# Kernel tuning notes

Measured on AMD Instinct MI355X. Metric: run time of the kernel, lower is better.

Reference implementation:

```python
import jax, jax.numpy as jnp
import numpy as np

# ---- config (from init_kwargs) ----
IMG_SIZE = (4096.0, 4096.0)
MAP_SIZE = (256, 256)
BASE_SIZE = 16
RATIOS = np.array([0.5, 1.0, 2.0], dtype=np.float64)
SCALES = np.array([8.0, 16.0, 32.0], dtype=np.float64)
FEAT_STRIDE = 16
RPN_MIN_SIZE = 16.0
PRE_NMS_N = 12000
POST_NMS_N = 2000
NMS_THRESH = 0.7


def _generate_anchors():
    base = np.array([1, 1, BASE_SIZE, BASE_SIZE], dtype=np.float64) - 1
    w = base[2] - base[0] + 1
    h = base[3] - base[1] + 1
    cx = base[0] + 0.5 * (w - 1)
    cy = base[1] + 0.5 * (h - 1)
    size = w * h
    ws = np.round(np.sqrt(size / RATIOS))
    hs = np.round(ws * RATIOS)
    ratio_anchors = np.stack([cx - 0.5 * (ws - 1), cy - 0.5 * (hs - 1),
                              cx + 0.5 * (ws - 1), cy + 0.5 * (hs - 1)], axis=1)
    out = []
    for a in ratio_anchors:
        aw = a[2] - a[0] + 1
        ah = a[3] - a[1] + 1
        acx = a[0] + 0.5 * (aw - 1)
        acy = a[1] + 0.5 * (ah - 1)
        ws2 = aw * SCALES
        hs2 = ah * SCALES
        out.append(np.stack([acx - 0.5 * (ws2 - 1), acy - 0.5 * (hs2 - 1),
                             acx + 0.5 * (ws2 - 1), acy + 0.5 * (hs2 - 1)], axis=1))
    return np.concatenate(out, axis=0).astype(np.float32)  # [A=9, 4]


def _all_anchors():
    A = _generate_anchors()
    H, W = MAP_SIZE
    sx = np.arange(W) * FEAT_STRIDE
    sy = np.arange(H) * FEAT_STRIDE
    sx, sy = np.meshgrid(sx, sy)
    shifts = np.stack([sx.ravel(), sy.ravel(), sx.ravel(), sy.ravel()], axis=1).astype(np.float32)  # [K,4]
    return (shifts[:, None, :] + A[None, :, :]).reshape(-1, 4)  # [K*A, 4]


_ALL_ANCHORS = _all_anchors()  # [N, 4] constant


def setup_inputs() -> dict:
    key = jax.random.key(0)
    k1, k2 = jax.random.split(key)
    n = _ALL_ANCHORS.shape[0]
    delta = jax.random.normal(k1, (1, n, 4), dtype=jnp.float32) * 0.1
    score = jax.random.uniform(k2, (1, n, 2), dtype=jnp.float32)
    return {"delta": delta, "score": score}


def _proposal_forward(delta, score):
    anchors = jnp.asarray(_ALL_ANCHORS)  # [N,4]
    d = delta[0]                         # [N,4]
    s = score[0, :, 1]                   # [N]

    widths = anchors[:, 2] - anchors[:, 0] + 1.0
    heights = anchors[:, 3] - anchors[:, 1] + 1.0
    ctr_x = anchors[:, 0] + 0.5 * widths
    ctr_y = anchors[:, 1] + 0.5 * heights
    pcx = d[:, 0] * widths + ctr_x
    pcy = d[:, 1] * heights + ctr_y
    pw = jnp.exp(d[:, 2]) * widths
    ph = jnp.exp(d[:, 3]) * heights
    x0 = jnp.clip(pcx - 0.5 * pw, 0.0, IMG_SIZE[0])
    y0 = jnp.clip(pcy - 0.5 * ph, 0.0, IMG_SIZE[1])
    x1 = jnp.clip(pcx + 0.5 * pw, 0.0, IMG_SIZE[0])
    y1 = jnp.clip(pcy + 0.5 * ph, 0.0, IMG_SIZE[1])
    props = jnp.stack([x0, y0, x1, y1], axis=1)  # [N,4]

    # min-size filter: mask instead of dynamic gather (jit-friendly)
    w = props[:, 2] - props[:, 0]
    h = props[:, 3] - props[:, 1]
    valid = (w >= RPN_MIN_SIZE) & (h >= RPN_MIN_SIZE)
    s = jnp.where(valid, s, -jnp.inf)

    top_s, top_i = jax.lax.top_k(s, PRE_NMS_N)   # sorted descending
    boxes = props[top_i]                          # [PRE,4]

    # greedy NMS over score-sorted boxes, fixed POST_NMS_N iterations
    areas = (boxes[:, 2] - boxes[:, 0]) * (boxes[:, 3] - boxes[:, 1])
    alive0 = top_s > -jnp.inf

    def step(alive, _):
        i = jnp.argmax(jnp.where(alive, top_s, -jnp.inf))
        ok = alive[i]
        b = boxes[i]
        xx0 = jnp.maximum(b[0], boxes[:, 0])
        yy0 = jnp.maximum(b[1], boxes[:, 1])
        xx1 = jnp.minimum(b[2], boxes[:, 2])
        yy1 = jnp.minimum(b[3], boxes[:, 3])
        inter = jnp.maximum(xx1 - xx0, 0.0) * jnp.maximum(yy1 - yy0, 0.0)
        iou = inter / jnp.maximum(areas[i] + areas - inter, 1e-8)
        alive = alive & (iou <= NMS_THRESH)
        out = jnp.where(ok, b, jnp.zeros_like(b))  # zero-pad like tf.pad
        return alive, out

    _, selected = jax.lax.scan(step, alive0, None, length=POST_NMS_N)  # [POST,4]
    return selected[None]  # [1, POST_NMS_N, 4]


def reference(delta, score):
    return _proposal_forward(delta, score)
```

## Files before the change

### kernel.cpp

```cpp
#include <hip/hip_runtime.h>
#include <hip/hip_bf16.h>

#define N_ANCH   589824
#define NBLK     2304
#define TOPK     12000
#define KPAD     12032
#define NW       188
#define OUTN     2000
#define CAP      32768
#define NBIN     65536

typedef unsigned long long u64;

__constant__ float c_aw[9] = {184.f, 368.f, 736.f, 128.f, 256.f, 512.f,  88.f, 176.f, 352.f};
__constant__ float c_ah[9] = { 96.f, 192.f, 384.f, 128.f, 256.f, 512.f, 176.f, 352.f, 704.f};

__device__ __forceinline__ void decode_one(int i, const float4* __restrict__ delta,
                                           float4* box, bool* valid) {
#pragma clang fp contract(off)
    int a    = i % 9;
    int cell = i / 9;
    int gx = cell & 255;
    int gy = cell >> 8;
    float w = c_aw[a], h = c_ah[a];
    float cx = (float)gx * 16.0f + 8.0f;
    float cy = (float)gy * 16.0f + 8.0f;
    float4 d = delta[i];
    float pcx = d.x * w + cx;
    float pcy = d.y * h + cy;
    float pw  = expf(d.z) * w;
    float ph  = expf(d.w) * h;
    float x0 = fminf(fmaxf(pcx - 0.5f * pw, 0.f), 4096.f);
    float y0 = fminf(fmaxf(pcy - 0.5f * ph, 0.f), 4096.f);
    float x1 = fminf(fmaxf(pcx + 0.5f * pw, 0.f), 4096.f);
    float y1 = fminf(fmaxf(pcy + 0.5f * ph, 0.f), 4096.f);
    *box = make_float4(x0, y0, x1, y1);
    *valid = (x1 - x0 >= 16.f) && (y1 - y0 >= 16.f);
}

__global__ __launch_bounds__(256) void k_score(const float4* __restrict__ delta,
                                               const float2* __restrict__ score,
                                               unsigned* __restrict__ ukey,
                                               unsigned* __restrict__ hist,
                                               unsigned* __restrict__ ctrl) {
    int tid = threadIdx.x;
    int i = blockIdx.x * 256 + tid;
    float4 box; bool valid;
    decode_one(i, delta, &box, &valid);
    unsigned u = 0u;
    if (valid) {
        unsigned b = __float_as_uint(score[i].y);
        u = (b & 0x80000000u) ? ~b : (b | 0x80000000u);
    }
    ukey[i] = u;
    atomicAdd(&hist[u >> 16], 1u);

    __shared__ int lastf;
    __threadfence();
    __syncthreads();
    if (tid == 0) lastf = (atomicAdd(&ctrl[8], 1u) == (unsigned)(gridDim.x - 1)) ? 1 : 0;
    __syncthreads();
    if (!lastf) return;

    __shared__ unsigned ss[256];
    __shared__ int sc;
    unsigned csum = 0;
    const unsigned* hb = hist + tid * 256;
    #pragma unroll 8
    for (int k = 0; k < 256; ++k) csum += hb[k];
    ss[tid] = csum;
    if (tid == 0) sc = -1;
    __syncthreads();
    for (int d = 1; d < 256; d <<= 1) {
        unsigned v = (tid + d < 256) ? ss[tid + d] : 0u;
        __syncthreads();
        ss[tid] += v;
        __syncthreads();
    }
    unsigned nextS = (tid + 1 < 256) ? ss[tid + 1] : 0u;
    if (ss[tid] >= (unsigned)TOPK && nextS < (unsigned)TOPK) sc = tid;
    __syncthreads();
    if (tid == 0) {
        unsigned P = 0;
        int c = sc;
        if (c >= 0) {
            unsigned acc = (c + 1 < 256) ? ss[c + 1] : 0u;
            int b = 255;
            for (; b > 0; --b) {
                acc += hist[c * 256 + b];
                if (acc >= (unsigned)TOPK) break;
            }
            P = (unsigned)(c * 256 + b);
        }
        ctrl[0] = P;
    }
}

__global__ __launch_bounds__(256) void k_compact(const unsigned* __restrict__ ukey,
                                                 const unsigned* __restrict__ ctrl,
                                                 unsigned* __restrict__ cnt,
                                                 u64* __restrict__ cand) {
    unsigned P = ctrl[0];
    int i = blockIdx.x * 256 + threadIdx.x;
    unsigned u = ukey[i];
    bool pred = (u != 0u) && ((u >> 16) >= P);
    u64 m = __ballot(pred);
    if (m == 0ull) return;
    int lane = threadIdx.x & 63;
    int leader = __ffsll(m) - 1;
    unsigned base = 0;
    if (lane == leader) base = atomicAdd(cnt, (unsigned)__popcll(m));
    base = __shfl(base, leader);
    if (pred) {
        u64 below = m & ((1ull << lane) - 1ull);
        unsigned pos = base + (unsigned)__popcll(below);
        if (pos < CAP) cand[pos] = ((u64)u << 32) | (unsigned)(~i);
    }
}

__global__ __launch_bounds__(256) void k_rankdec(const u64* __restrict__ cand,
                                                 const unsigned* __restrict__ ctrl,
                                                 const float4* __restrict__ delta,
                                                 float4* __restrict__ sboxes) {
    unsigned cnt = ctrl[3];
    int C = (int)(cnt < (unsigned)CAP ? cnt : (unsigned)CAP);
    if ((int)(blockIdx.x * 256) >= C) return;
    int t = blockIdx.x * 256 + threadIdx.x;
    u64 mykey = (t < C) ? cand[t] : ~0ull;
    int rank = 0;
    __shared__ u64 tile[256];
    for (int j0 = 0; j0 < C; j0 += 256) {
        int j = j0 + threadIdx.x;
        tile[threadIdx.x] = (j < C) ? cand[j] : 0ull;
        __syncthreads();
        int lim = (C - j0 < 256) ? (C - j0) : 256;
        #pragma unroll 4
        for (int jj = 0; jj < lim; ++jj) rank += (tile[jj] > mykey) ? 1 : 0;
        __syncthreads();
    }
    if (t < C && rank < TOPK) {
        int idx = (int)(~(unsigned)mykey);
        float4 box; bool v;
        decode_one(idx, delta, &box, &v);
        sboxes[rank] = box;
    }
}

__global__ __launch_bounds__(64) void k_mask(const float4* __restrict__ sboxes,
                                             u64* __restrict__ mask) {
    int cb = blockIdx.x, rb = blockIdx.y;
    if (cb < rb) return;
    __shared__ float4 cbox[64];
    int tid = threadIdx.x;
    cbox[tid] = sboxes[cb * 64 + tid];
    __syncthreads();
    int r = rb * 64 + tid;
    float4 me = sboxes[r];
    float areaMe = (me.z - me.x) * (me.w - me.y);
    u64 bits = 0ull;
    for (int j = 0; j < 64; ++j) {
        float4 o = cbox[j];
        float xx0 = fmaxf(me.x, o.x);
        float yy0 = fmaxf(me.y, o.y);
        float xx1 = fminf(me.z, o.z);
        float yy1 = fminf(me.w, o.w);
        float iw = fmaxf(xx1 - xx0, 0.f);
        float ih = fmaxf(yy1 - yy0, 0.f);
        float inter = iw * ih;
        float areaO = (o.z - o.x) * (o.w - o.y);
        float denom = fmaxf(areaMe + areaO - inter, 1e-8f);
        float iou = inter / denom;
        if (iou > 0.7f && (cb * 64 + j) != r) bits |= (1ull << j);
    }
    mask[(size_t)r * NW + cb] = bits;
}

__global__ __launch_bounds__(256) void k_reduce(const float4* __restrict__ sboxes,
                                                const unsigned* __restrict__ ctrl,
                                                const u64* __restrict__ mask,
                                                float4* __restrict__ out) {
    int t = threadIdx.x;
    int lane = t & 63;
    int wave = t >> 6;
    unsigned cnt = ctrl[3];
    int C = (int)(cnt < (unsigned)CAP ? cnt : (unsigned)CAP);
    int nvalid = C < TOPK ? C : TOPK;
    int nblocks = (nvalid + 63) >> 6;

    __shared__ u64 diag[2][64];
    __shared__ u64 s_rw;
    __shared__ unsigned s_rows[64];
    __shared__ int s_kc;
    __shared__ int s_nkept;

    u64 removed_t = ~0ull;
    if (t < NW) {
        long long lo = (long long)t * 64;
        if (lo + 64 <= (long long)nvalid) removed_t = 0ull;
        else if (lo < (long long)nvalid)
            removed_t = ~((1ull << (unsigned)(nvalid - lo)) - 1ull);
    }
    if (t == 0) s_nkept = 0;
    if (wave == 3 && nblocks > 0) diag[0][lane] = mask[(size_t)lane * NW + 0];
    __syncthreads();

    for (int b = 0; b < nblocks; ++b) {
        int cur = b & 1;
        if (wave == 3 && b + 1 < nblocks)
            diag[cur ^ 1][lane] = mask[(size_t)((b + 1) * 64 + lane) * NW + (b + 1)];
        if (t == b) s_rw = removed_t;
        __syncthreads();

        if (wave == 0) {
            u64 dg = diag[cur][lane];
            u64 avail = ~s_rw;
            int nk = s_nkept;
            int budget = OUTN - nk;
            u64 keptmask = 0ull; int kc = 0;
            while (avail && kc < budget) {
                int j = __ffsll(avail) - 1;
                keptmask |= (1ull << j);
                ++kc;
                u64 dj = __shfl(dg, j);
                avail &= ~dj;
                avail &= ~(1ull << j);
            }
            if ((keptmask >> lane) & 1ull) {
                int p = (int)__popcll(keptmask & ((1ull << lane) - 1ull));
                s_rows[p] = (unsigned)(b * 64 + lane);
                out[nk + p] = sboxes[b * 64 + lane];
            }
            if (kc > 0) {
                int r0 = b * 64 + (__ffsll(keptmask) - 1);
                int kcp = (kc + 7) & ~7;
                if (lane >= kc && lane < kcp) s_rows[lane] = (unsigned)r0;
            }
            if (lane == 0) { s_kc = kc; s_nkept = nk + kc; }
        }
        __syncthreads();

        if (s_nkept >= OUTN) break;
        int kc = s_kc;
        if (kc > 0 && t < NW && t > b) {
            const u64* mt = mask + t;
            u64 acc = removed_t;
            int kcp = (kc + 7) & ~7;
            for (int i = 0; i < kcp; i += 8) {
                u64 a0 = mt[(size_t)s_rows[i + 0] * NW];
                u64 a1 = mt[(size_t)s_rows[i + 1] * NW];
                u64 a2 = mt[(size_t)s_rows[i + 2] * NW];
                u64 a3 = mt[(size_t)s_rows[i + 3] * NW];
                u64 a4 = mt[(size_t)s_rows[i + 4] * NW];
                u64 a5 = mt[(size_t)s_rows[i + 5] * NW];
                u64 a6 = mt[(size_t)s_rows[i + 6] * NW];
                u64 a7 = mt[(size_t)s_rows[i + 7] * NW];
                acc |= ((a0 | a1) | (a2 | a3)) | ((a4 | a5) | (a6 | a7));
            }
            removed_t = acc;
        }
    }

    int nk = s_nkept;
    float4 z = make_float4(0.f, 0.f, 0.f, 0.f);
    for (int p = nk + t; p < OUTN; p += 256) out[p] = z;
}

extern "C" void kernel_launch(void* const* d_in, const int* in_sizes, int n_in,
                              void* d_out, int out_size, void* d_ws, size_t ws_size,
                              hipStream_t stream) {
    const float4* delta = (const float4*)d_in[0];
    const float2* score = (const float2*)d_in[1];
    char* ws = (char*)d_ws;

    unsigned* ukey = (unsigned*)(ws + 0);
    unsigned* hist = (unsigned*)(ws + 2359296);
    u64*      cand = (u64*)(ws + 2359296);
    unsigned* ctrl = (unsigned*)(ws + 2621440);
    float4*   sbox = (float4*)(ws + 2621504);
    u64*      mask = (u64*)(ws + 2814016);

    hipMemsetAsync(ws + 2359296, 0, 262144 + 64, stream);
    hipMemsetAsync(ws + 2621504, 0, 192512, stream);

    k_score  <<<NBLK,     256, 0, stream>>>(delta, score, ukey, hist, ctrl);
    k_compact<<<NBLK,     256, 0, stream>>>(ukey, ctrl, ctrl + 3, cand);
    k_rankdec<<<CAP/256,  256, 0, stream>>>(cand, ctrl, delta, sbox);
    dim3 mgrid(NW, NW);
    k_mask   <<<mgrid,    64,  0, stream>>>(sbox, mask);
    k_reduce <<<1,        256, 0, stream>>>(sbox, ctrl, mask, (float4*)d_out);
}
```

Baseline: 1.037 ms.

## Split histogram threshold into own kernel, coarsen mask blocks, widen reduce unroll

Moves the last-block histogram scan out of k_score into a separate 1024-thread k_thresh kernel that reads the histogram with vectorized uint4 loads. This removes the per-block threadfence and atomic counter from k_score, at the cost of one extra launch. k_mask now has each block handle four column tiles, cutting launch count and skipped empty blocks. k_reduce unrolls its mask OR loop to 16 loads so more memory requests are in flight, but pads kept rows to multiples of 16, which can add redundant loads.

```diff
diff --git a/kernel.cpp b/kernel.cpp
--- a/kernel.cpp
+++ b/kernel.cpp
@@ -8,7 +8,6 @@
 #define NW       188
 #define OUTN     2000
 #define CAP      32768
-#define NBIN     65536
 
 typedef unsigned long long u64;
 
@@ -41,10 +40,8 @@
 __global__ __launch_bounds__(256) void k_score(const float4* __restrict__ delta,
                                                const float2* __restrict__ score,
                                                unsigned* __restrict__ ukey,
-                                               unsigned* __restrict__ hist,
-                                               unsigned* __restrict__ ctrl) {
-    int tid = threadIdx.x;
-    int i = blockIdx.x * 256 + tid;
+                                               unsigned* __restrict__ hist) {
+    int i = blockIdx.x * 256 + threadIdx.x;
     float4 box; bool valid;
     decode_one(i, delta, &box, &valid);
     unsigned u = 0u;
@@ -54,43 +51,43 @@
     }
     ukey[i] = u;
     atomicAdd(&hist[u >> 16], 1u);
-
-    __shared__ int lastf;
-    __threadfence();
-    __syncthreads();
-    if (tid == 0) lastf = (atomicAdd(&ctrl[8], 1u) == (unsigned)(gridDim.x - 1)) ? 1 : 0;
-    __syncthreads();
-    if (!lastf) return;
-
-    __shared__ unsigned ss[256];
+}
+
+__global__ __launch_bounds__(1024) void k_thresh(const unsigned* __restrict__ hist,
+                                                 unsigned* __restrict__ ctrl) {
+    __shared__ unsigned ss[1024];
     __shared__ int sc;
+    int tid = threadIdx.x;
+    const uint4* hb = (const uint4*)hist + tid * 16;
     unsigned csum = 0;
-    const unsigned* hb = hist + tid * 256;
-    #pragma unroll 8
-    for (int k = 0; k < 256; ++k) csum += hb[k];
+    #pragma unroll
+    for (int k = 0; k < 16; ++k) {
+        uint4 h = hb[k];
+        csum += h.x + h.y + h.z + h.w;
+    }
     ss[tid] = csum;
     if (tid == 0) sc = -1;
     __syncthreads();
-    for (int d = 1; d < 256; d <<= 1) {
-        unsigned v = (tid + d < 256) ? ss[tid + d] : 0u;
+    for (int d = 1; d < 1024; d <<= 1) {
+        unsigned v = (tid + d < 1024) ? ss[tid + d] : 0u;
         __syncthreads();
         ss[tid] += v;
         __syncthreads();
     }
-    unsigned nextS = (tid + 1 < 256) ? ss[tid + 1] : 0u;
+    unsigned nextS = (tid + 1 < 1024) ? ss[tid + 1] : 0u;
     if (ss[tid] >= (unsigned)TOPK && nextS < (unsigned)TOPK) sc = tid;
     __syncthreads();
     if (tid == 0) {
         unsigned P = 0;
         int c = sc;
         if (c >= 0) {
-            unsigned acc = (c + 1 < 256) ? ss[c + 1] : 0u;
-            int b = 255;
+            unsigned acc = (c + 1 < 1024) ? ss[c + 1] : 0u;
+            int b = 63;
             for (; b > 0; --b) {
-                acc += hist[c * 256 + b];
+                acc += hist[c * 64 + b];
                 if (acc >= (unsigned)TOPK) break;
             }
-            P = (unsigned)(c * 256 + b);
+            P = (unsigned)(c * 64 + b);
         }
         ctrl[0] = P;
     }
@@ -148,31 +145,37 @@
 
 __global__ __launch_bounds__(64) void k_mask(const float4* __restrict__ sboxes,
                                              u64* __restrict__ mask) {
-    int cb = blockIdx.x, rb = blockIdx.y;
-    if (cb < rb) return;
-    __shared__ float4 cbox[64];
+    int rb = blockIdx.y;
+    int cb0 = blockIdx.x * 4;
+    if (cb0 + 3 < rb) return;
     int tid = threadIdx.x;
-    cbox[tid] = sboxes[cb * 64 + tid];
-    __syncthreads();
     int r = rb * 64 + tid;
     float4 me = sboxes[r];
     float areaMe = (me.z - me.x) * (me.w - me.y);
-    u64 bits = 0ull;
-    for (int j = 0; j < 64; ++j) {
-        float4 o = cbox[j];
-        float xx0 = fmaxf(me.x, o.x);
-        float yy0 = fmaxf(me.y, o.y);
-        float xx1 = fminf(me.z, o.z);
-        float yy1 = fminf(me.w, o.w);
-        float iw = fmaxf(xx1 - xx0, 0.f);
-        float ih = fmaxf(yy1 - yy0, 0.f);
-        float inter = iw * ih;
-        float areaO = (o.z - o.x) * (o.w - o.y);
-        float denom = fmaxf(areaMe + areaO - inter, 1e-8f);
-        float iou = inter / denom;
-        if (iou > 0.7f && (cb * 64 + j) != r) bits |= (1ull << j);
-    }
-    mask[(size_t)r * NW + cb] = bits;
+    __shared__ float4 cbox[64];
+    for (int q = 0; q < 4; ++q) {
+        int cb = cb0 + q;
+        if (cb < rb) continue;
+        __syncthreads();
+        cbox[tid] = sboxes[cb * 64 + tid];
+        __syncthreads();
+        u64 bits = 0ull;
+        for (int j = 0; j < 64; ++j) {
+            float4 o = cbox[j];
+            float xx0 = fmaxf(me.x, o.x);
+            float yy0 = fmaxf(me.y, o.y);
+            float xx1 = fminf(me.z, o.z);
+            float yy1 = fminf(me.w, o.w);
+            float iw = fmaxf(xx1 - xx0, 0.f);
+            float ih = fmaxf(yy1 - yy0, 0.f);
+            float inter = iw * ih;
+            float areaO = (o.z - o.x) * (o.w - o.y);
+            float denom = fmaxf(areaMe + areaO - inter, 1e-8f);
+            float iou = inter / denom;
+            if (iou > 0.7f && (cb * 64 + j) != r) bits |= (1ull << j);
+        }
+        mask[(size_t)r * NW + cb] = bits;
+    }
 }
 
 __global__ __launch_bounds__(256) void k_reduce(const float4* __restrict__ sboxes,
@@ -232,7 +235,7 @@
             }
             if (kc > 0) {
                 int r0 = b * 64 + (__ffsll(keptmask) - 1);
-                int kcp = (kc + 7) & ~7;
+                int kcp = (kc + 15) & ~15;
                 if (lane >= kc && lane < kcp) s_rows[lane] = (unsigned)r0;
             }
             if (lane == 0) { s_kc = kc; s_nkept = nk + kc; }
@@ -244,17 +247,26 @@
         if (kc > 0 && t < NW && t > b) {
             const u64* mt = mask + t;
             u64 acc = removed_t;
-            int kcp = (kc + 7) & ~7;
-            for (int i = 0; i < kcp; i += 8) {
-                u64 a0 = mt[(size_t)s_rows[i + 0] * NW];
-                u64 a1 = mt[(size_t)s_rows[i + 1] * NW];
-                u64 a2 = mt[(size_t)s_rows[i + 2] * NW];
-                u64 a3 = mt[(size_t)s_rows[i + 3] * NW];
-                u64 a4 = mt[(size_t)s_rows[i + 4] * NW];
-                u64 a5 = mt[(size_t)s_rows[i + 5] * NW];
-                u64 a6 = mt[(size_t)s_rows[i + 6] * NW];
-                u64 a7 = mt[(size_t)s_rows[i + 7] * NW];
-                acc |= ((a0 | a1) | (a2 | a3)) | ((a4 | a5) | (a6 | a7));
+            int kcp = (kc + 15) & ~15;
+            for (int i = 0; i < kcp; i += 16) {
+                u64 a0  = mt[(size_t)s_rows[i + 0]  * NW];
+                u64 a1  = mt[(size_t)s_rows[i + 1]  * NW];
+                u64 a2  = mt[(size_t)s_rows[i + 2]  * NW];
+                u64 a3  = mt[(size_t)s_rows[i + 3]  * NW];
+                u64 a4  = mt[(size_t)s_rows[i + 4]  * NW];
+                u64 a5  = mt[(size_t)s_rows[i + 5]  * NW];
+                u64 a6  = mt[(size_t)s_rows[i + 6]  * NW];
+                u64 a7  = mt[(size_t)s_rows[i + 7]  * NW];
+                u64 a8  = mt[(size_t)s_rows[i + 8]  * NW];
+                u64 a9  = mt[(size_t)s_rows[i + 9]  * NW];
+                u64 a10 = mt[(size_t)s_rows[i + 10] * NW];
+                u64 a11 = mt[(size_t)s_rows[i + 11] * NW];
+                u64 a12 = mt[(size_t)s_rows[i + 12] * NW];
+                u64 a13 = mt[(size_t)s_rows[i + 13] * NW];
+                u64 a14 = mt[(size_t)s_rows[i + 14] * NW];
+                u64 a15 = mt[(size_t)s_rows[i + 15] * NW];
+                acc |= (((a0 | a1) | (a2 | a3)) | ((a4 | a5) | (a6 | a7)))
+                     | (((a8 | a9) | (a10 | a11)) | ((a12 | a13) | (a14 | a15)));
             }
             removed_t = acc;
         }
@@ -282,10 +294,11 @@
     hipMemsetAsync(ws + 2359296, 0, 262144 + 64, stream);
     hipMemsetAsync(ws + 2621504, 0, 192512, stream);
 
-    k_score  <<<NBLK,     256, 0, stream>>>(delta, score, ukey, hist, ctrl);
-    k_compact<<<NBLK,     256, 0, stream>>>(ukey, ctrl, ctrl + 3, cand);
-    k_rankdec<<<CAP/256,  256, 0, stream>>>(cand, ctrl, delta, sbox);
-    dim3 mgrid(NW, NW);
-    k_mask   <<<mgrid,    64,  0, stream>>>(sbox, mask);
-    k_reduce <<<1,        256, 0, stream>>>(sbox, ctrl, mask, (float4*)d_out);
-}
+    k_score  <<<NBLK,    256,  0, stream>>>(delta, score, ukey, hist);
+    k_thresh <<<1,       1024, 0, stream>>>(hist, ctrl);
+    k_compact<<<NBLK,    256,  0, stream>>>(ukey, ctrl, ctrl + 3, cand);
+    k_rankdec<<<CAP/256, 256,  0, stream>>>(cand, ctrl, delta, sbox);
+    dim3 mgrid(47, NW);
+    k_mask   <<<mgrid,   64,   0, stream>>>(sbox, mask);
+    k_reduce <<<1,       256,  0, stream>>>(sbox, ctrl, mask, (float4*)d_out);
+}
```

Measured after the change: 985.1 us. 1.05x faster.

## Two-pass LDS radix histogram, column-major NMS mask, and barrier-light reduce loop

Applied to the files above, without the earlier changes.

Replaces the 65536-bin global-atomic histogram and last-block threshold search with two 256-bin passes that aggregate counts in shared memory first, adding a k_hist2 kernel. Each block of k_compact recomputes the threshold from the two histograms. The NMS mask becomes column-major, and each k_mask block computes four column tiles. k_reduce runs the intra-block greedy pass with ballot in all waves, so it needs one barrier per block instead of two, and it prefetches the kept-row mask words into registers. The cost is an extra launch and redundant prefix scans in every compact block.

```diff
diff --git a/kernel.cpp b/kernel.cpp
--- a/kernel.cpp
+++ b/kernel.cpp
@@ -8,7 +8,6 @@
 #define NW       188
 #define OUTN     2000
 #define CAP      32768
-#define NBIN     65536
 
 typedef unsigned long long u64;
 
@@ -41,9 +40,11 @@
 __global__ __launch_bounds__(256) void k_score(const float4* __restrict__ delta,
                                                const float2* __restrict__ score,
                                                unsigned* __restrict__ ukey,
-                                               unsigned* __restrict__ hist,
-                                               unsigned* __restrict__ ctrl) {
+                                               unsigned* __restrict__ hist1) {
+    __shared__ unsigned lh[256];
     int tid = threadIdx.x;
+    lh[tid] = 0u;
+    __syncthreads();
     int i = blockIdx.x * 256 + tid;
     float4 box; bool valid;
     decode_one(i, delta, &box, &valid);
@@ -53,23 +54,22 @@
         u = (b & 0x80000000u) ? ~b : (b | 0x80000000u);
     }
     ukey[i] = u;
-    atomicAdd(&hist[u >> 16], 1u);
-
-    __shared__ int lastf;
-    __threadfence();
-    __syncthreads();
-    if (tid == 0) lastf = (atomicAdd(&ctrl[8], 1u) == (unsigned)(gridDim.x - 1)) ? 1 : 0;
-    __syncthreads();
-    if (!lastf) return;
-
+    atomicAdd(&lh[u >> 24], 1u);
+    __syncthreads();
+    unsigned c = lh[tid];
+    if (c) atomicAdd(&hist1[tid], c);
+}
+
+__global__ __launch_bounds__(256) void k_hist2(const unsigned* __restrict__ ukey,
+                                               const unsigned* __restrict__ hist1,
+                                               unsigned* __restrict__ hist2) {
     __shared__ unsigned ss[256];
-    __shared__ int sc;
-    unsigned csum = 0;
-    const unsigned* hb = hist + tid * 256;
-    #pragma unroll 8
-    for (int k = 0; k < 256; ++k) csum += hb[k];
-    ss[tid] = csum;
-    if (tid == 0) sc = -1;
+    __shared__ unsigned lh[256];
+    __shared__ unsigned s_b1;
+    int tid = threadIdx.x;
+    ss[tid] = hist1[tid];
+    lh[tid] = 0u;
+    if (tid == 0) s_b1 = 0u;
     __syncthreads();
     for (int d = 1; d < 256; d <<= 1) {
         unsigned v = (tid + d < 256) ? ss[tid + d] : 0u;
@@ -77,36 +77,62 @@
         ss[tid] += v;
         __syncthreads();
     }
-    unsigned nextS = (tid + 1 < 256) ? ss[tid + 1] : 0u;
-    if (ss[tid] >= (unsigned)TOPK && nextS < (unsigned)TOPK) sc = tid;
-    __syncthreads();
-    if (tid == 0) {
-        unsigned P = 0;
-        int c = sc;
-        if (c >= 0) {
-            unsigned acc = (c + 1 < 256) ? ss[c + 1] : 0u;
-            int b = 255;
-            for (; b > 0; --b) {
-                acc += hist[c * 256 + b];
-                if (acc >= (unsigned)TOPK) break;
-            }
-            P = (unsigned)(c * 256 + b);
-        }
-        ctrl[0] = P;
-    }
+    if (ss[tid] >= (unsigned)TOPK && (tid == 255 || ss[tid + 1] < (unsigned)TOPK))
+        s_b1 = (unsigned)tid;
+    __syncthreads();
+    unsigned b1 = s_b1;
+    int i = blockIdx.x * 256 + tid;
+    unsigned u = ukey[i];
+    if ((u >> 24) == b1) atomicAdd(&lh[(u >> 16) & 255u], 1u);
+    __syncthreads();
+    unsigned c = lh[tid];
+    if (c) atomicAdd(&hist2[tid], c);
 }
 
 __global__ __launch_bounds__(256) void k_compact(const unsigned* __restrict__ ukey,
-                                                 const unsigned* __restrict__ ctrl,
+                                                 const unsigned* __restrict__ hist1,
+                                                 const unsigned* __restrict__ hist2,
                                                  unsigned* __restrict__ cnt,
                                                  u64* __restrict__ cand) {
-    unsigned P = ctrl[0];
-    int i = blockIdx.x * 256 + threadIdx.x;
+    __shared__ unsigned ss[256];
+    __shared__ unsigned s_b1, s_ab1, s_P;
+    int tid = threadIdx.x;
+    ss[tid] = hist1[tid];
+    if (tid == 0) { s_b1 = 0u; s_ab1 = 0u; }
+    __syncthreads();
+    for (int d = 1; d < 256; d <<= 1) {
+        unsigned v = (tid + d < 256) ? ss[tid + d] : 0u;
+        __syncthreads();
+        ss[tid] += v;
+        __syncthreads();
+    }
+    if (ss[tid] >= (unsigned)TOPK && (tid == 255 || ss[tid + 1] < (unsigned)TOPK)) {
+        s_b1 = (unsigned)tid;
+        s_ab1 = (tid == 255) ? 0u : ss[tid + 1];
+    }
+    __syncthreads();
+    unsigned b1 = s_b1, ab1 = s_ab1;
+    ss[tid] = hist2[tid];
+    if (tid == 0) s_P = (b1 << 8);
+    __syncthreads();
+    for (int d = 1; d < 256; d <<= 1) {
+        unsigned v = (tid + d < 256) ? ss[tid + d] : 0u;
+        __syncthreads();
+        ss[tid] += v;
+        __syncthreads();
+    }
+    unsigned target = (unsigned)TOPK - ab1;
+    if (ss[tid] >= target && (tid == 255 || ss[tid + 1] < target))
+        s_P = (b1 << 8) | (unsigned)tid;
+    __syncthreads();
+    unsigned P = s_P;
+
+    int i = blockIdx.x * 256 + tid;
     unsigned u = ukey[i];
     bool pred = (u != 0u) && ((u >> 16) >= P);
     u64 m = __ballot(pred);
     if (m == 0ull) return;
-    int lane = threadIdx.x & 63;
+    int lane = tid & 63;
     int leader = __ffsll(m) - 1;
     unsigned base = 0;
     if (lane == leader) base = atomicAdd(cnt, (unsigned)__popcll(m));
@@ -147,37 +173,43 @@
 }
 
 __global__ __launch_bounds__(64) void k_mask(const float4* __restrict__ sboxes,
-                                             u64* __restrict__ mask) {
-    int cb = blockIdx.x, rb = blockIdx.y;
-    if (cb < rb) return;
-    __shared__ float4 cbox[64];
+                                             u64* __restrict__ mcol) {
+    int rb = blockIdx.y;
+    int cb0 = blockIdx.x * 4;
+    if (cb0 + 3 < rb) return;
     int tid = threadIdx.x;
-    cbox[tid] = sboxes[cb * 64 + tid];
-    __syncthreads();
     int r = rb * 64 + tid;
     float4 me = sboxes[r];
     float areaMe = (me.z - me.x) * (me.w - me.y);
-    u64 bits = 0ull;
-    for (int j = 0; j < 64; ++j) {
-        float4 o = cbox[j];
-        float xx0 = fmaxf(me.x, o.x);
-        float yy0 = fmaxf(me.y, o.y);
-        float xx1 = fminf(me.z, o.z);
-        float yy1 = fminf(me.w, o.w);
-        float iw = fmaxf(xx1 - xx0, 0.f);
-        float ih = fmaxf(yy1 - yy0, 0.f);
-        float inter = iw * ih;
-        float areaO = (o.z - o.x) * (o.w - o.y);
-        float denom = fmaxf(areaMe + areaO - inter, 1e-8f);
-        float iou = inter / denom;
-        if (iou > 0.7f && (cb * 64 + j) != r) bits |= (1ull << j);
-    }
-    mask[(size_t)r * NW + cb] = bits;
+    __shared__ float4 cbox[64];
+    for (int q = 0; q < 4; ++q) {
+        int cb = cb0 + q;
+        if (cb < rb) continue;
+        __syncthreads();
+        cbox[tid] = sboxes[cb * 64 + tid];
+        __syncthreads();
+        u64 bits = 0ull;
+        for (int j = 0; j < 64; ++j) {
+            float4 o = cbox[j];
+            float xx0 = fmaxf(me.x, o.x);
+            float yy0 = fmaxf(me.y, o.y);
+            float xx1 = fminf(me.z, o.z);
+            float yy1 = fminf(me.w, o.w);
+            float iw = fmaxf(xx1 - xx0, 0.f);
+            float ih = fmaxf(yy1 - yy0, 0.f);
+            float inter = iw * ih;
+            float areaO = (o.z - o.x) * (o.w - o.y);
+            float denom = fmaxf(areaMe + areaO - inter, 1e-8f);
+            float iou = inter / denom;
+            if (iou > 0.7f && (cb * 64 + j) != r) bits |= (1ull << j);
+        }
+        mcol[(size_t)cb * KPAD + r] = bits;
+    }
 }
 
 __global__ __launch_bounds__(256) void k_reduce(const float4* __restrict__ sboxes,
                                                 const unsigned* __restrict__ ctrl,
-                                                const u64* __restrict__ mask,
+                                                const u64* __restrict__ mcol,
                                                 float4* __restrict__ out) {
     int t = threadIdx.x;
     int lane = t & 63;
@@ -187,11 +219,7 @@
     int nvalid = C < TOPK ? C : TOPK;
     int nblocks = (nvalid + 63) >> 6;
 
-    __shared__ u64 diag[2][64];
-    __shared__ u64 s_rw;
-    __shared__ unsigned s_rows[64];
-    __shared__ int s_kc;
-    __shared__ int s_nkept;
+    __shared__ u64 s_rw[2];
 
     u64 removed_t = ~0ull;
     if (t < NW) {
@@ -200,67 +228,76 @@
         else if (lo < (long long)nvalid)
             removed_t = ~((1ull << (unsigned)(nvalid - lo)) - 1ull);
     }
-    if (t == 0) s_nkept = 0;
-    if (wave == 3 && nblocks > 0) diag[0][lane] = mask[(size_t)lane * NW + 0];
-    __syncthreads();
+
+    int nk = 0;
+    u64 p0=0,p1=0,p2=0,p3=0,p4=0,p5=0,p6=0,p7=0;
+    u64 p8=0,p9=0,p10=0,p11=0,p12=0,p13=0,p14=0,p15=0;
+    u64 dgnext = 0ull;
+    if (nblocks > 0) dgnext = mcol[(size_t)0 * KPAD + lane];
 
     for (int b = 0; b < nblocks; ++b) {
-        int cur = b & 1;
-        if (wave == 3 && b + 1 < nblocks)
-            diag[cur ^ 1][lane] = mask[(size_t)((b + 1) * 64 + lane) * NW + (b + 1)];
-        if (t == b) s_rw = removed_t;
-        __syncthreads();
-
-        if (wave == 0) {
-            u64 dg = diag[cur][lane];
-            u64 avail = ~s_rw;
-            int nk = s_nkept;
-            int budget = OUTN - nk;
-            u64 keptmask = 0ull; int kc = 0;
-            while (avail && kc < budget) {
-                int j = __ffsll(avail) - 1;
-                keptmask |= (1ull << j);
-                ++kc;
-                u64 dj = __shfl(dg, j);
-                avail &= ~dj;
-                avail &= ~(1ull << j);
+        removed_t |= ((p0|p1)|(p2|p3)) | ((p4|p5)|(p6|p7));
+        removed_t |= ((p8|p9)|(p10|p11)) | ((p12|p13)|(p14|p15));
+        p0=p1=p2=p3=p4=p5=p6=p7=0ull;
+        p8=p9=p10=p11=p12=p13=p14=p15=0ull;
+        u64 dg = dgnext;
+        if (t == b) s_rw[b & 1] = removed_t;
+        __syncthreads();
+        u64 rw = s_rw[b & 1];
+        if (b + 1 < nblocks)
+            dgnext = mcol[(size_t)(b + 1) * KPAD + (size_t)(b + 1) * 64 + lane];
+
+        bool alive = ((rw >> lane) & 1ull) == 0ull;
+        int budget = OUTN - nk;
+        u64 keptmask = 0ull;
+        int kc = 0;
+        while (kc < budget) {
+            u64 m = __ballot(alive);
+            if (!m) break;
+            int j = __ffsll(m) - 1;
+            keptmask |= (1ull << j);
+            ++kc;
+            alive = alive && (lane != j) && (((dg >> j) & 1ull) == 0ull);
+        }
+
+        if (wave == 0 && ((keptmask >> lane) & 1ull)) {
+            int pos = nk + (int)__popcll(keptmask & ((1ull << lane) - 1ull));
+            out[pos] = sboxes[b * 64 + lane];
+        }
+        nk += kc;
+        if (nk >= OUTN) break;
+
+        if (kc > 0 && t > b && t < NW) {
+            const u64* colp = mcol + (size_t)t * KPAD + (size_t)b * 64;
+            u64 km = keptmask;
+            int jf = __ffsll(km) - 1;
+            int i0 = jf;                          km &= km - 1;
+            int i1  = km ? __ffsll(km) - 1 : jf;  km &= km - 1;
+            int i2  = km ? __ffsll(km) - 1 : jf;  km &= km - 1;
+            int i3  = km ? __ffsll(km) - 1 : jf;  km &= km - 1;
+            int i4  = km ? __ffsll(km) - 1 : jf;  km &= km - 1;
+            int i5  = km ? __ffsll(km) - 1 : jf;  km &= km - 1;
+            int i6  = km ? __ffsll(km) - 1 : jf;  km &= km - 1;
+            int i7  = km ? __ffsll(km) - 1 : jf;  km &= km - 1;
+            int i8  = km ? __ffsll(km) - 1 : jf;  km &= km - 1;
+            int i9  = km ? __ffsll(km) - 1 : jf;  km &= km - 1;
+            int i10 = km ? __ffsll(km) - 1 : jf;  km &= km - 1;
+            int i11 = km ? __ffsll(km) - 1 : jf;  km &= km - 1;
+            int i12 = km ? __ffsll(km) - 1 : jf;  km &= km - 1;
+            int i13 = km ? __ffsll(km) - 1 : jf;  km &= km - 1;
+            int i14 = km ? __ffsll(km) - 1 : jf;  km &= km - 1;
+            int i15 = km ? __ffsll(km) - 1 : jf;  km &= km - 1;
+            p0 = colp[i0];   p1 = colp[i1];   p2 = colp[i2];   p3 = colp[i3];
+            p4 = colp[i4];   p5 = colp[i5];   p6 = colp[i6];   p7 = colp[i7];
+            p8 = colp[i8];   p9 = colp[i9];   p10 = colp[i10]; p11 = colp[i11];
+            p12 = colp[i12]; p13 = colp[i13]; p14 = colp[i14]; p15 = colp[i15];
+            while (km) {
+                int j = __ffsll(km) - 1; km &= km - 1;
+                removed_t |= colp[j];
             }
-            if ((keptmask >> lane) & 1ull) {
-                int p = (int)__popcll(keptmask & ((1ull << lane) - 1ull));
-                s_rows[p] = (unsigned)(b * 64 + lane);
-                out[nk + p] = sboxes[b * 64 + lane];
-            }
-            if (kc > 0) {
-                int r0 = b * 64 + (__ffsll(keptmask) - 1);
-                int kcp = (kc + 7) & ~7;
-                if (lane >= kc && lane < kcp) s_rows[lane] = (unsigned)r0;
-            }
-            if (lane == 0) { s_kc = kc; s_nkept = nk + kc; }
         }
-        __syncthreads();
-
-        if (s_nkept >= OUTN) break;
-        int kc = s_kc;
-        if (kc > 0 && t < NW && t > b) {
-            const u64* mt = mask + t;
-            u64 acc = removed_t;
-            int kcp = (kc + 7) & ~7;
-            for (int i = 0; i < kcp; i += 8) {
-                u64 a0 = mt[(size_t)s_rows[i + 0] * NW];
-                u64 a1 = mt[(size_t)s_rows[i + 1] * NW];
-                u64 a2 = mt[(size_t)s_rows[i + 2] * NW];
-                u64 a3 = mt[(size_t)s_rows[i + 3] * NW];
-                u64 a4 = mt[(size_t)s_rows[i + 4] * NW];
-                u64 a5 = mt[(size_t)s_rows[i + 5] * NW];
-                u64 a6 = mt[(size_t)s_rows[i + 6] * NW];
-                u64 a7 = mt[(size_t)s_rows[i + 7] * NW];
-                acc |= ((a0 | a1) | (a2 | a3)) | ((a4 | a5) | (a6 | a7));
-            }
-            removed_t = acc;
-        }
-    }
-
-    int nk = s_nkept;
+    }
+
     float4 z = make_float4(0.f, 0.f, 0.f, 0.f);
     for (int p = nk + t; p < OUTN; p += 256) out[p] = z;
 }
@@ -272,20 +309,21 @@
     const float2* score = (const float2*)d_in[1];
     char* ws = (char*)d_ws;
 
-    unsigned* ukey = (unsigned*)(ws + 0);
-    unsigned* hist = (unsigned*)(ws + 2359296);
-    u64*      cand = (u64*)(ws + 2359296);
-    unsigned* ctrl = (unsigned*)(ws + 2621440);
-    float4*   sbox = (float4*)(ws + 2621504);
-    u64*      mask = (u64*)(ws + 2814016);
-
-    hipMemsetAsync(ws + 2359296, 0, 262144 + 64, stream);
-    hipMemsetAsync(ws + 2621504, 0, 192512, stream);
-
-    k_score  <<<NBLK,     256, 0, stream>>>(delta, score, ukey, hist, ctrl);
-    k_compact<<<NBLK,     256, 0, stream>>>(ukey, ctrl, ctrl + 3, cand);
-    k_rankdec<<<CAP/256,  256, 0, stream>>>(cand, ctrl, delta, sbox);
-    dim3 mgrid(NW, NW);
-    k_mask   <<<mgrid,    64,  0, stream>>>(sbox, mask);
-    k_reduce <<<1,        256, 0, stream>>>(sbox, ctrl, mask, (float4*)d_out);
-}
+    unsigned* ukey  = (unsigned*)(ws + 0);
+    u64*      cand  = (u64*)(ws + 2359296);
+    unsigned* hist1 = (unsigned*)(ws + 2621440);
+    unsigned* hist2 = (unsigned*)(ws + 2622464);
+    unsigned* ctrl  = (unsigned*)(ws + 2623488);
+    float4*   sbox  = (float4*)(ws + 2623552);
+    u64*      mcol  = (u64*)(ws + 2816064);
+
+    hipMemsetAsync(ws + 2621440, 0, 194624, stream);
+
+    k_score  <<<NBLK,    256, 0, stream>>>(delta, score, ukey, hist1);
+    k_hist2  <<<NBLK,    256, 0, stream>>>(ukey, hist1, hist2);
+    k_compact<<<NBLK,    256, 0, stream>>>(ukey, hist1, hist2, ctrl + 3, cand);
+    k_rankdec<<<CAP/256, 256, 0, stream>>>(cand, ctrl, delta, sbox);
+    dim3 mgrid(47, NW);
+    k_mask   <<<mgrid,   64,  0, stream>>>(sbox, mcol);
+    k_reduce <<<1,       256, 0, stream>>>(sbox, ctrl, mcol, (float4*)d_out);
+}
```

After: 891.0 us. 1.16x faster.
